# Kernel optimization log

Hardware: AMD Instinct MI355X
Metric: run time of the kernel (lower is better)

The kernel has to match this reference:

```python
import jax, jax.numpy as jnp
import numpy as np

ROPE_BASE = 10000.0


def _apply_rope(q, k, start_pos):
    # q, k: (B, T, H, D) with half-split (LLaMA-style) rotation
    B, T, H, D = q.shape
    half = D // 2
    inv_freq = 1.0 / (ROPE_BASE ** (jnp.arange(0, half, dtype=jnp.float32) / half))
    pos = (start_pos + jnp.arange(T)).astype(jnp.float32)
    ang = pos[:, None] * inv_freq[None, :]          # (T, half)
    cos = jnp.cos(ang)[None, :, None, :]            # (1, T, 1, half)
    sin = jnp.sin(ang)[None, :, None, :]

    def rot(t):
        t1, t2 = t[..., :half], t[..., half:]
        return jnp.concatenate([t1 * cos - t2 * sin, t1 * sin + t2 * cos], axis=-1)

    return rot(q), rot(k)


def setup_inputs() -> dict:
    key = jax.random.key(0)
    k1, k2, k3 = jax.random.split(key, 3)
    B, T, C = 2, 2048, 2048
    x = jax.random.normal(k1, (B, T, C), dtype=jnp.float32)
    # torch Linear weights: (out_features, in_features), scaled like default init
    Wqkv = jax.random.normal(k2, (3 * C, C), dtype=jnp.float32) * (C ** -0.5)
    Wproj = jax.random.normal(k3, (C, C), dtype=jnp.float32) * (C ** -0.5)
    return {"x": x, "Wqkv": Wqkv, "Wproj": Wproj, "start_pos": 0}


def reference(x, Wqkv, Wproj, start_pos):
    B, T, C = x.shape
    H = 16
    D = C // H
    scale = D ** -0.5

    qkv = x @ Wqkv.T                                 # (B, T, 3C)
    q, k, v = jnp.split(qkv, 3, axis=-1)
    q = q.reshape(B, T, H, D)
    k = k.reshape(B, T, H, D)
    v = v.reshape(B, T, H, D)
    q, k = _apply_rope(q, k, start_pos)

    att = jnp.einsum("bthd,bshd->bhts", q, k) * scale   # (B, H, T, T)
    causal = jnp.tril(jnp.ones((T, T), dtype=bool))
    att = jnp.where(causal[None, None], att, -jnp.inf)
    att = jax.nn.softmax(att, axis=-1)
    out = jnp.einsum("bhts,bshd->bthd", att, v)          # (B, T, H, D)
    out = out.reshape(B, T, C)
    return out @ Wproj.T
```

## Files before the change

kernel.cpp:

```cpp
#include <hip/hip_runtime.h>
#include <hip/hip_bf16.h>
#include <stdint.h>
#include <math.h>

#define B_    2
#define T_    2048
#define C_    2048
#define H_    16
#define D_    128
#define NQKV  6144
#define BT_   4096

typedef __attribute__((ext_vector_type(8))) short  short8;
typedef __attribute__((ext_vector_type(4))) short  short4_;
typedef __attribute__((ext_vector_type(4))) float  float4_;

__device__ __forceinline__ unsigned short f2bf(float f) {
  union { float f; unsigned int u; } v; v.f = f;
  unsigned int u = v.u;
  return (unsigned short)((u + 0x7FFFu + ((u >> 16) & 1u)) >> 16);
}
__device__ __forceinline__ float bf2f(unsigned short u) {
  union { unsigned int i; float f; } v; v.i = ((unsigned int)u) << 16;
  return v.f;
}
__device__ __forceinline__ void pk2(short4_& dst, int idx2, float a, float b) {
  union { __hip_bfloat162 h2; struct { short x, y; } s; } u;
  u.h2 = __float22bfloat162_rn(make_float2(a, b));
  dst[idx2 * 2]     = u.s.x;
  dst[idx2 * 2 + 1] = u.s.y;
}

__device__ __forceinline__ void async_cp16(const unsigned short* g, unsigned short* l) {
  __builtin_amdgcn_global_load_lds((__attribute__((address_space(1))) void*)g,
                                   (__attribute__((address_space(3))) void*)l,
                                   16, 0, 0);
}

__global__ __launch_bounds__(256) void cvt_all(const float* __restrict__ x,
                                               const float* __restrict__ wqkv,
                                               const float* __restrict__ wproj,
                                               const int* __restrict__ sp_ptr,
                                               unsigned short* __restrict__ out,
                                               float* __restrict__ ct,
                                               float* __restrict__ st) {
  if (blockIdx.x >= 12288) {
    int j = (blockIdx.x - 12288) * 256 + threadIdx.x;
    int d = j & 63;
    const float L2F = -0.20762050593046013f;
    float fr = exp2f((float)d * L2F);
    float ang = (float)(sp_ptr[0] + (j >> 6)) * fr;
    ct[j] = cosf(ang);
    st[j] = sinf(ang);
    return;
  }
  int i = (blockIdx.x * 256 + threadIdx.x) * 8;
  const float* src; int off;
  if (i < 8388608)       { src = x;     off = i; }
  else if (i < 20971520) { src = wqkv;  off = i - 8388608; }
  else                   { src = wproj; off = i - 20971520; }
  const float4_* p = (const float4_*)(src + off);
  float4_ a = p[0], b = p[1];
  short8 o;
  o[0] = (short)f2bf(a[0]); o[1] = (short)f2bf(a[1]);
  o[2] = (short)f2bf(a[2]); o[3] = (short)f2bf(a[3]);
  o[4] = (short)f2bf(b[0]); o[5] = (short)f2bf(b[1]);
  o[6] = (short)f2bf(b[2]); o[7] = (short)f2bf(b[3]);
  *(short8*)(out + i) = o;
}

template <bool F32OUT>
__global__ __launch_bounds__(256) void gemm_bt(const unsigned short* __restrict__ A,
                                               const unsigned short* __restrict__ Bm,
                                               void* __restrict__ Cout,
                                               int M, int N, int K) {
  __shared__ __align__(16) unsigned short As[128 * 64];
  __shared__ __align__(16) unsigned short Bs[128 * 64];
  const int tid  = threadIdx.x;
  const int lane = tid & 63;
  const int col16 = lane & 15, quad = lane >> 4;
  const int wave = tid >> 6;
  const int wm = wave >> 1, wn = wave & 1;
  const int m0 = blockIdx.y * 128, n0 = blockIdx.x * 128;

  float4_ acc[4][4] = {};

  #pragma unroll 1
  for (int k0 = 0; k0 < K; k0 += 64) {
    __syncthreads();
    #pragma unroll
    for (int i = 0; i < 4; ++i) {
      int P   = i * 256 + tid;
      int row = P >> 3;
      int kc  = (P & 7) ^ (row & 7);
      async_cp16(A  + (size_t)(m0 + row) * K + k0 + kc * 8, As + P * 8);
      async_cp16(Bm + (size_t)(n0 + row) * K + k0 + kc * 8, Bs + P * 8);
    }
    __syncthreads();
    #pragma unroll
    for (int ks = 0; ks < 2; ++ks) {
      short8 af[4], bf[4];
      #pragma unroll
      for (int i = 0; i < 4; ++i) {
        int ra = wm * 64 + i * 16 + col16;
        int ca = ((ks * 4 + quad) ^ (ra & 7)) * 8;
        af[i] = *(const short8*)(As + ra * 64 + ca);
        int rb = wn * 64 + i * 16 + col16;
        int cb = ((ks * 4 + quad) ^ (rb & 7)) * 8;
        bf[i] = *(const short8*)(Bs + rb * 64 + cb);
      }
      #pragma unroll
      for (int i = 0; i < 4; ++i)
        #pragma unroll
        for (int j = 0; j < 4; ++j)
          acc[i][j] = __builtin_amdgcn_mfma_f32_16x16x32_bf16(af[i], bf[j], acc[i][j], 0, 0, 0);
    }
  }

  #pragma unroll
  for (int i = 0; i < 4; ++i) {
    int mg = m0 + wm * 64 + i * 16 + quad * 4;
    #pragma unroll
    for (int j = 0; j < 4; ++j) {
      int ng = n0 + wn * 64 + j * 16 + col16;
      #pragma unroll
      for (int r = 0; r < 4; ++r) {
        if constexpr (F32OUT)
          ((float*)Cout)[(size_t)(mg + r) * N + ng] = acc[i][j][r];
        else
          ((unsigned short*)Cout)[(size_t)(mg + r) * N + ng] = f2bf(acc[i][j][r]);
      }
    }
  }
}

__global__ __launch_bounds__(256) void gemm_qkv(const unsigned short* __restrict__ A,
                                                const unsigned short* __restrict__ Bm,
                                                const float* __restrict__ ct,
                                                const float* __restrict__ st,
                                                unsigned short* __restrict__ q_r,
                                                unsigned short* __restrict__ k_r,
                                                unsigned short* __restrict__ v_t) {
  __shared__ __align__(16) unsigned short S[16384];
  unsigned short* As = S;
  unsigned short* Bs = S + 8192;
  const int tid  = threadIdx.x;
  const int lane = tid & 63;
  const int col16 = lane & 15, quad = lane >> 4;
  const int wave = tid >> 6;
  const int wm = wave >> 1, wn = wave & 1;
  const int m0 = blockIdx.y * 128, n0 = blockIdx.x * 128;

  float4_ acc[4][4] = {};

  #pragma unroll 1
  for (int k0 = 0; k0 < C_; k0 += 64) {
    __syncthreads();
    #pragma unroll
    for (int i = 0; i < 4; ++i) {
      int P   = i * 256 + tid;
      int row = P >> 3;
      int kc  = (P & 7) ^ (row & 7);
      async_cp16(A  + (size_t)(m0 + row) * C_ + k0 + kc * 8, As + P * 8);
      async_cp16(Bm + (size_t)(n0 + row) * C_ + k0 + kc * 8, Bs + P * 8);
    }
    __syncthreads();
    #pragma unroll
    for (int ks = 0; ks < 2; ++ks) {
      short8 af[4], bf[4];
      #pragma unroll
      for (int i = 0; i < 4; ++i) {
        int ra = wm * 64 + i * 16 + col16;
        int ca = ((ks * 4 + quad) ^ (ra & 7)) * 8;
        af[i] = *(const short8*)(As + ra * 64 + ca);
        int rb = wn * 32 + (i & 1) * 16 + (i >> 1) * 64 + col16;
        int cb = ((ks * 4 + quad) ^ (rb & 7)) * 8;
        bf[i] = *(const short8*)(Bs + rb * 64 + cb);
      }
      #pragma unroll
      for (int i = 0; i < 4; ++i)
        #pragma unroll
        for (int j = 0; j < 4; ++j)
          acc[i][j] = __builtin_amdgcn_mfma_f32_16x16x32_bf16(af[i], bf[j], acc[i][j], 0, 0, 0);
    }
  }

  const int region = n0 >> 11;
  const int h   = (n0 & 2047) >> 7;
  const int b   = m0 >> 11;
  const int t0l = m0 & 2047;
  const int bh  = b * H_ + h;

  if (region < 2) {
    unsigned short* dst = region ? k_r : q_r;
    const float scl = region ? 1.0f : 0.1275174117f;
    #pragma unroll
    for (int i = 0; i < 4; ++i) {
      int tl = t0l + wm * 64 + i * 16 + quad * 4;
      #pragma unroll
      for (int jl = 0; jl < 2; ++jl) {
        int d = wn * 32 + jl * 16 + col16;
        size_t ob = (size_t)(bh * T_ + tl) * D_ + d;
        int ti = tl * 64 + d;
        #pragma unroll
        for (int r = 0; r < 4; ++r) {
          float cs = ct[ti + r * 64], sn = st[ti + r * 64];
          float lo = acc[i][jl][r], hi = acc[i][jl + 2][r];
          dst[ob + (size_t)r * D_]      = f2bf((lo * cs - hi * sn) * scl);
          dst[ob + (size_t)r * D_ + 64] = f2bf((lo * sn + hi * cs) * scl);
        }
      }
    }
  } else {
    __syncthreads();
    #pragma unroll
    for (int i = 0; i < 4; ++i) {
      int tlb = wm * 64 + i * 16 + quad * 4;
      #pragma unroll
      for (int j = 0; j < 4; ++j) {
        int d = wn * 32 + (j & 1) * 16 + (j >> 1) * 64 + col16;
        #pragma unroll
        for (int r = 0; r < 4; ++r) {
          int t = tlb + r;
          int ch = (t >> 3) ^ (d & 15);
          S[d * 128 + ch * 8 + (t & 7)] = f2bf(acc[i][j][r]);
        }
      }
    }
    __syncthreads();
    int drow = tid >> 1, hf = tid & 1;
    size_t gb = (size_t)(bh * D_ + drow) * T_ + t0l + hf * 64;
    #pragma unroll
    for (int cc = 0; cc < 8; ++cc) {
      int ch = (hf * 8 + cc) ^ (drow & 15);
      *(short8*)(v_t + gb + cc * 8) = *(const short8*)(S + drow * 128 + ch * 8);
    }
  }
}

__global__ __launch_bounds__(512, 4) void attn_fwd(const unsigned short* __restrict__ q_r,
                                                   const unsigned short* __restrict__ k_r,
                                                   const unsigned short* __restrict__ v_t,
                                                   unsigned short* __restrict__ Ob) {
  __shared__ __align__(16) unsigned short Ks[2][64 * 128];
  __shared__ __align__(16) unsigned short Vts[2][128 * 64];
  __shared__ __align__(16) unsigned short Ps[128 * 64];
  const int g     = blockIdx.x >> 5;
  const int bh    = blockIdx.x & 31;
  const int qt    = (g < 8) ? g : 23 - g;
  const int tid  = threadIdx.x;
  const int lane = tid & 63;
  const int col16 = lane & 15, quad = lane >> 4;
  const int wave = tid >> 6;
  const float NEG_INF = -__builtin_inff();
  const int b = bh >> 4, h = bh & 15;
  const int qlr = wave * 16 + col16;

  const int q0 = qt * 128;
  const int njt = 2 * qt + 2;

  short8 qf[4];
  const unsigned short* qp = q_r + (size_t)(bh * T_ + q0 + qlr) * D_;
  #pragma unroll
  for (int ks = 0; ks < 4; ++ks) qf[ks] = *(const short8*)(qp + ks * 32 + quad * 8);

  float4_ oacc[8] = {};
  float m_i = NEG_INF, l_i = 0.f;

  const unsigned short* kbase = k_r + (size_t)bh * T_ * D_;
  const unsigned short* vbase = v_t + (size_t)bh * D_ * T_;
  #define STAGE(JT, BUF)                                                        \
    {                                                                           \
      const unsigned short* kb = kbase + (size_t)(JT) * 64 * D_;                \
      const unsigned short* vb = vbase + (size_t)(JT) * 64;                     \
      unsigned short* kd = &Ks[(BUF)][0];                                       \
      unsigned short* vd = &Vts[(BUF)][0];                                      \
      _Pragma("unroll")                                                         \
      for (int i = 0; i < 2; ++i) {                                             \
        int P = i * 512 + tid;                                                  \
        int krow = P >> 4, kc = (P & 15) ^ (krow & 7);                          \
        async_cp16(kb + krow * D_ + kc * 8, kd + P * 8);                        \
        int vrow = P >> 3, vc = (P & 7) ^ (vrow & 7);                           \
        async_cp16(vb + (size_t)vrow * T_ + vc * 8, vd + P * 8);                \
      }                                                                         \
    }

  STAGE(0, 0);

  #pragma unroll 1
  for (int jt = 0; jt < njt; ++jt) {
    __syncthreads();
    if (jt + 1 < njt) STAGE(jt + 1, (jt + 1) & 1);

    if (jt * 64 > q0 + wave * 16 + 15) continue;

    const unsigned short* KsB  = &Ks[jt & 1][0];
    const unsigned short* VtsB = &Vts[jt & 1][0];

    float4_ s[4];
    #pragma unroll
    for (int jn = 0; jn < 4; ++jn) {
      float4_ a = {};
      #pragma unroll
      for (int ks = 0; ks < 4; ++ks) {
        int kr = jn * 16 + col16;
        int ch = ((ks * 4 + quad) ^ (kr & 7)) * 8;
        short8 kfr = *(const short8*)(KsB + kr * 128 + ch);
        a = __builtin_amdgcn_mfma_f32_16x16x32_bf16(kfr, qf[ks], a, 0, 0, 0);
      }
      s[jn] = a;
    }
    if (jt * 64 + 63 > q0 + wave * 16) {
      #pragma unroll
      for (int jn = 0; jn < 4; ++jn)
        #pragma unroll
        for (int r = 0; r < 4; ++r)
          if (jt * 64 + jn * 16 + quad * 4 + r > q0 + qlr) s[jn][r] = NEG_INF;
    }
    float rm = NEG_INF;
    #pragma unroll
    for (int jn = 0; jn < 4; ++jn)
      #pragma unroll
      for (int r = 0; r < 4; ++r) rm = fmaxf(rm, s[jn][r]);
    rm = fmaxf(rm, __shfl_xor(rm, 16));
    rm = fmaxf(rm, __shfl_xor(rm, 32));
    float m_new = fmaxf(m_i, rm);
    float alpha = exp2f(m_i - m_new);
    float rs = 0.f;
    #pragma unroll
    for (int jn = 0; jn < 4; ++jn)
      #pragma unroll
      for (int r = 0; r < 4; ++r) {
        float pv = exp2f(s[jn][r] - m_new);
        s[jn][r] = pv;
        rs += pv;
      }
    rs += __shfl_xor(rs, 16);
    rs += __shfl_xor(rs, 32);
    l_i = l_i * alpha + rs;
    m_i = m_new;
    #pragma unroll
    for (int dt = 0; dt < 8; ++dt) oacc[dt] *= alpha;

    #pragma unroll
    for (int jn = 0; jn < 4; ++jn) {
      short4_ pkv;
      pk2(pkv, 0, s[jn][0], s[jn][1]);
      pk2(pkv, 1, s[jn][2], s[jn][3]);
      int c0 = jn * 16 + quad * 4;
      int ch = (c0 >> 3) ^ (qlr & 7);
      *(short4_*)(Ps + qlr * 64 + ch * 8 + (c0 & 7)) = pkv;
    }
    __builtin_amdgcn_s_waitcnt(0xC07F);

    short8 pf[2];
    #pragma unroll
    for (int ks2 = 0; ks2 < 2; ++ks2) {
      int ch = ((ks2 * 4 + quad) ^ (qlr & 7)) * 8;
      pf[ks2] = *(const short8*)(Ps + qlr * 64 + ch);
    }
    #pragma unroll
    for (int dt = 0; dt < 8; ++dt)
      #pragma unroll
      for (int ks2 = 0; ks2 < 2; ++ks2) {
        int vr = dt * 16 + col16;
        int ch = ((ks2 * 4 + quad) ^ (vr & 7)) * 8;
        short8 vf = *(const short8*)(VtsB + vr * 64 + ch);
        oacc[dt] = __builtin_amdgcn_mfma_f32_16x16x32_bf16(vf, pf[ks2], oacc[dt], 0, 0, 0);
      }
  }

  float inv_l = 1.0f / l_i;
  size_t ob = (size_t)(b * T_ + q0 + qlr) * C_ + h * D_;
  #pragma unroll
  for (int dt = 0; dt < 8; ++dt) {
    short4_ o4;
    pk2(o4, 0, oacc[dt][0] * inv_l, oacc[dt][1] * inv_l);
    pk2(o4, 1, oacc[dt][2] * inv_l, oacc[dt][3] * inv_l);
    *(short4_*)(Ob + ob + dt * 16 + quad * 4) = o4;
  }
  #undef STAGE
}

extern "C" void kernel_launch(void* const* d_in, const int* in_sizes, int n_in,
                              void* d_out, int out_size, void* d_ws, size_t ws_size,
                              hipStream_t stream) {
  const float* x     = (const float*)d_in[0];
  const float* Wqkv  = (const float*)d_in[1];
  const float* Wproj = (const float*)d_in[2];
  const int*   sp    = (const int*)d_in[3];
  float* out = (float*)d_out;

  unsigned short* ws     = (unsigned short*)d_ws;
  unsigned short* xb     = ws;
  unsigned short* wqkvb  = xb + 8388608;
  unsigned short* wprojb = wqkvb + 12582912;
  unsigned short* q_r    = wprojb + 4194304;
  unsigned short* k_r    = q_r + 8388608;
  unsigned short* v_t    = k_r + 8388608;
  float*          ctab   = (float*)(v_t + 8388608);
  float*          stab   = ctab + 131072;
  unsigned short* Obuf   = xb;

  cvt_all<<<12800, 256, 0, stream>>>(x, Wqkv, Wproj, sp, ws, ctab, stab);

  gemm_qkv<<<dim3(48, 32), 256, 0, stream>>>(xb, wqkvb, ctab, stab, q_r, k_r, v_t);

  attn_fwd<<<dim3(512), 512, 0, stream>>>(q_r, k_r, v_t, Obuf);

  gemm_bt<true><<<dim3(16, 32), 256, 0, stream>>>(Obuf, wprojb, (void*)out, BT_, C_, C_);
}
```

Measured before the change: 366.1 us.

## Switch attention to 32x32x16 MFMA with 4 waves of 32 query rows

The attention kernel moves from 16x16x32 to 32x32x16 bf16 MFMA. The block shrinks from 8 to 4 waves, each owning 32 query rows instead of 16, and fragment layouts, masking, the P writeback and the output store are remapped to match. Larger MFMA tiles cut LDS fragment reads per FLOP and drop one cross-lane shuffle step in the softmax reductions. In exchange, register pressure rises (16-float accumulators), fewer waves are resident per block, and each thread does more staging copies.

Result: slower. 379.3 us (+3.6%).

```diff
diff --git a/kernel.cpp b/kernel.cpp
--- a/kernel.cpp
+++ b/kernel.cpp
@@ -11,9 +11,10 @@
 #define NQKV  6144
 #define BT_   4096
 
-typedef __attribute__((ext_vector_type(8))) short  short8;
-typedef __attribute__((ext_vector_type(4))) short  short4_;
-typedef __attribute__((ext_vector_type(4))) float  float4_;
+typedef __attribute__((ext_vector_type(8)))  short short8;
+typedef __attribute__((ext_vector_type(4)))  short short4_;
+typedef __attribute__((ext_vector_type(4)))  float float4_;
+typedef __attribute__((ext_vector_type(16))) float f32x16;
 
 __device__ __forceinline__ unsigned short f2bf(float f) {
   union { float f; unsigned int u; } v; v.f = f;
@@ -238,10 +239,10 @@
   }
 }
 
-__global__ __launch_bounds__(512, 4) void attn_fwd(const unsigned short* __restrict__ q_r,
-                                                   const unsigned short* __restrict__ k_r,
-                                                   const unsigned short* __restrict__ v_t,
-                                                   unsigned short* __restrict__ Ob) {
+__global__ __launch_bounds__(256) void attn_fwd(const unsigned short* __restrict__ q_r,
+                                                const unsigned short* __restrict__ k_r,
+                                                const unsigned short* __restrict__ v_t,
+                                                unsigned short* __restrict__ Ob) {
   __shared__ __align__(16) unsigned short Ks[2][64 * 128];
   __shared__ __align__(16) unsigned short Vts[2][128 * 64];
   __shared__ __align__(16) unsigned short Ps[128 * 64];
@@ -250,21 +251,22 @@
   const int qt    = (g < 8) ? g : 23 - g;
   const int tid  = threadIdx.x;
   const int lane = tid & 63;
-  const int col16 = lane & 15, quad = lane >> 4;
-  const int wave = tid >> 6;
+  const int l31  = lane & 31;
+  const int hi   = lane >> 5;
+  const int w    = tid >> 6;
   const float NEG_INF = -__builtin_inff();
   const int b = bh >> 4, h = bh & 15;
-  const int qlr = wave * 16 + col16;
+  const int qlr = w * 32 + l31;
 
   const int q0 = qt * 128;
   const int njt = 2 * qt + 2;
 
-  short8 qf[4];
+  short8 qf[8];
   const unsigned short* qp = q_r + (size_t)(bh * T_ + q0 + qlr) * D_;
   #pragma unroll
-  for (int ks = 0; ks < 4; ++ks) qf[ks] = *(const short8*)(qp + ks * 32 + quad * 8);
-
-  float4_ oacc[8] = {};
+  for (int ks = 0; ks < 8; ++ks) qf[ks] = *(const short8*)(qp + ks * 16 + hi * 8);
+
+  f32x16 oacc[4] = {};
   float m_i = NEG_INF, l_i = 0.f;
 
   const unsigned short* kbase = k_r + (size_t)bh * T_ * D_;
@@ -276,8 +278,8 @@
       unsigned short* kd = &Ks[(BUF)][0];                                       \
       unsigned short* vd = &Vts[(BUF)][0];                                      \
       _Pragma("unroll")                                                         \
-      for (int i = 0; i < 2; ++i) {                                             \
-        int P = i * 512 + tid;                                                  \
+      for (int i = 0; i < 4; ++i) {                                             \
+        int P = i * 256 + tid;                                                  \
         int krow = P >> 4, kc = (P & 15) ^ (krow & 7);                          \
         async_cp16(kb + krow * D_ + kc * 8, kd + P * 8);                        \
         int vrow = P >> 3, vc = (P & 7) ^ (vrow & 7);                           \
@@ -292,93 +294,97 @@
     __syncthreads();
     if (jt + 1 < njt) STAGE(jt + 1, (jt + 1) & 1);
 
-    if (jt * 64 > q0 + wave * 16 + 15) continue;
+    if (jt * 64 > q0 + w * 32 + 31) continue;
 
     const unsigned short* KsB  = &Ks[jt & 1][0];
     const unsigned short* VtsB = &Vts[jt & 1][0];
 
-    float4_ s[4];
-    #pragma unroll
-    for (int jn = 0; jn < 4; ++jn) {
-      float4_ a = {};
-      #pragma unroll
-      for (int ks = 0; ks < 4; ++ks) {
-        int kr = jn * 16 + col16;
-        int ch = ((ks * 4 + quad) ^ (kr & 7)) * 8;
+    f32x16 s32[2];
+    #pragma unroll
+    for (int jn = 0; jn < 2; ++jn) {
+      f32x16 a = {};
+      #pragma unroll
+      for (int ks = 0; ks < 8; ++ks) {
+        int kr = jn * 32 + l31;
+        int ch = ((ks * 2 + hi) ^ (kr & 7)) * 8;
         short8 kfr = *(const short8*)(KsB + kr * 128 + ch);
-        a = __builtin_amdgcn_mfma_f32_16x16x32_bf16(kfr, qf[ks], a, 0, 0, 0);
-      }
-      s[jn] = a;
-    }
-    if (jt * 64 + 63 > q0 + wave * 16) {
-      #pragma unroll
-      for (int jn = 0; jn < 4; ++jn)
+        a = __builtin_amdgcn_mfma_f32_32x32x16_bf16(kfr, qf[ks], a, 0, 0, 0);
+      }
+      s32[jn] = a;
+    }
+    if (jt * 64 + 63 > q0 + w * 32) {
+      #pragma unroll
+      for (int jn = 0; jn < 2; ++jn)
         #pragma unroll
-        for (int r = 0; r < 4; ++r)
-          if (jt * 64 + jn * 16 + quad * 4 + r > q0 + qlr) s[jn][r] = NEG_INF;
+        for (int reg = 0; reg < 16; ++reg) {
+          int mrow = (reg & 3) + 8 * (reg >> 2) + 4 * hi;
+          if (jt * 64 + jn * 32 + mrow > q0 + qlr) s32[jn][reg] = NEG_INF;
+        }
     }
     float rm = NEG_INF;
     #pragma unroll
-    for (int jn = 0; jn < 4; ++jn)
-      #pragma unroll
-      for (int r = 0; r < 4; ++r) rm = fmaxf(rm, s[jn][r]);
-    rm = fmaxf(rm, __shfl_xor(rm, 16));
+    for (int jn = 0; jn < 2; ++jn)
+      #pragma unroll
+      for (int reg = 0; reg < 16; ++reg) rm = fmaxf(rm, s32[jn][reg]);
     rm = fmaxf(rm, __shfl_xor(rm, 32));
     float m_new = fmaxf(m_i, rm);
     float alpha = exp2f(m_i - m_new);
     float rs = 0.f;
     #pragma unroll
-    for (int jn = 0; jn < 4; ++jn)
-      #pragma unroll
-      for (int r = 0; r < 4; ++r) {
-        float pv = exp2f(s[jn][r] - m_new);
-        s[jn][r] = pv;
+    for (int jn = 0; jn < 2; ++jn)
+      #pragma unroll
+      for (int reg = 0; reg < 16; ++reg) {
+        float pv = exp2f(s32[jn][reg] - m_new);
+        s32[jn][reg] = pv;
         rs += pv;
       }
-    rs += __shfl_xor(rs, 16);
     rs += __shfl_xor(rs, 32);
     l_i = l_i * alpha + rs;
     m_i = m_new;
     #pragma unroll
-    for (int dt = 0; dt < 8; ++dt) oacc[dt] *= alpha;
-
-    #pragma unroll
-    for (int jn = 0; jn < 4; ++jn) {
-      short4_ pkv;
-      pk2(pkv, 0, s[jn][0], s[jn][1]);
-      pk2(pkv, 1, s[jn][2], s[jn][3]);
-      int c0 = jn * 16 + quad * 4;
-      int ch = (c0 >> 3) ^ (qlr & 7);
-      *(short4_*)(Ps + qlr * 64 + ch * 8 + (c0 & 7)) = pkv;
-    }
+    for (int dt = 0; dt < 4; ++dt) oacc[dt] *= alpha;
+
+    #pragma unroll
+    for (int jn = 0; jn < 2; ++jn)
+      #pragma unroll
+      for (int gg = 0; gg < 4; ++gg) {
+        short4_ pkv;
+        pk2(pkv, 0, s32[jn][gg * 4 + 0], s32[jn][gg * 4 + 1]);
+        pk2(pkv, 1, s32[jn][gg * 4 + 2], s32[jn][gg * 4 + 3]);
+        int chv = (jn * 4 + gg) ^ (qlr & 7);
+        *(short4_*)(Ps + qlr * 64 + chv * 8 + hi * 4) = pkv;
+      }
     __builtin_amdgcn_s_waitcnt(0xC07F);
 
-    short8 pf[2];
-    #pragma unroll
-    for (int ks2 = 0; ks2 < 2; ++ks2) {
-      int ch = ((ks2 * 4 + quad) ^ (qlr & 7)) * 8;
-      pf[ks2] = *(const short8*)(Ps + qlr * 64 + ch);
-    }
-    #pragma unroll
-    for (int dt = 0; dt < 8; ++dt)
-      #pragma unroll
-      for (int ks2 = 0; ks2 < 2; ++ks2) {
-        int vr = dt * 16 + col16;
-        int ch = ((ks2 * 4 + quad) ^ (vr & 7)) * 8;
+    short8 pfv[4];
+    #pragma unroll
+    for (int ks2 = 0; ks2 < 4; ++ks2) {
+      int ch = ((ks2 * 2 + hi) ^ (qlr & 7)) * 8;
+      pfv[ks2] = *(const short8*)(Ps + qlr * 64 + ch);
+    }
+    #pragma unroll
+    for (int dt = 0; dt < 4; ++dt)
+      #pragma unroll
+      for (int ks2 = 0; ks2 < 4; ++ks2) {
+        int vr = dt * 32 + l31;
+        int ch = ((ks2 * 2 + hi) ^ (vr & 7)) * 8;
         short8 vf = *(const short8*)(VtsB + vr * 64 + ch);
-        oacc[dt] = __builtin_amdgcn_mfma_f32_16x16x32_bf16(vf, pf[ks2], oacc[dt], 0, 0, 0);
+        oacc[dt] = __builtin_amdgcn_mfma_f32_32x32x16_bf16(vf, pfv[ks2], oacc[dt], 0, 0, 0);
       }
   }
 
   float inv_l = 1.0f / l_i;
   size_t ob = (size_t)(b * T_ + q0 + qlr) * C_ + h * D_;
   #pragma unroll
-  for (int dt = 0; dt < 8; ++dt) {
-    short4_ o4;
-    pk2(o4, 0, oacc[dt][0] * inv_l, oacc[dt][1] * inv_l);
-    pk2(o4, 1, oacc[dt][2] * inv_l, oacc[dt][3] * inv_l);
-    *(short4_*)(Ob + ob + dt * 16 + quad * 4) = o4;
-  }
+  for (int dt = 0; dt < 4; ++dt)
+    #pragma unroll
+    for (int gg = 0; gg < 4; ++gg) {
+      int d = dt * 32 + 8 * gg + 4 * hi;
+      short4_ o4;
+      pk2(o4, 0, oacc[dt][gg * 4 + 0] * inv_l, oacc[dt][gg * 4 + 1] * inv_l);
+      pk2(o4, 1, oacc[dt][gg * 4 + 2] * inv_l, oacc[dt][gg * 4 + 3] * inv_l);
+      *(short4_*)(Ob + ob + d) = o4;
+    }
   #undef STAGE
 }
 
@@ -406,7 +412,7 @@
 
   gemm_qkv<<<dim3(48, 32), 256, 0, stream>>>(xb, wqkvb, ctab, stab, q_r, k_r, v_t);
 
-  attn_fwd<<<dim3(512), 512, 0, stream>>>(q_r, k_r, v_t, Obuf);
+  attn_fwd<<<dim3(512), 256, 0, stream>>>(q_r, k_r, v_t, Obuf);
 
   gemm_bt<true><<<dim3(16, 32), 256, 0, stream>>>(Obuf, wprojb, (void*)out, BT_, C_, C_);
 }
```
